# Kernel tuning notes

Hardware: AMD Instinct MI355X
Metric: run time of the kernel (lower is better)

Reference implementation:

```python
import jax, jax.numpy as jnp
import numpy as np


def setup_inputs() -> dict:
    key = jax.random.key(0)
    k1, k2 = jax.random.split(key)
    input = jax.random.normal(k1, (4, 2048, 2048), dtype=jnp.float32)
    target = jax.random.normal(k2, (4, 2048, 2048), dtype=jnp.float32) * 2.0 + 0.5
    return {"input": input, "target": target}


def _hist_match(source, template):
    """JAX histogram matching, equivalent to the numpy unique/cumsum/interp
    version for inputs with distinct values (true for continuous random data).

    For each source element x, its empirical quantile is
        q(x) = count(source <= x) / N  == s_quantiles[bin_idx] in the numpy code,
    computed via sort + searchsorted(side='right').
    The template CDF is the sorted template paired with quantiles (j+1)/M,
    matching cumsum(t_counts)/M at each (unique) value.
    """
    src = source.ravel()
    tmpl_sorted = jnp.sort(template.ravel())
    N = src.shape[0]
    M = tmpl_sorted.shape[0]
    s_sorted = jnp.sort(src)
    # rank of each element among all source elements (count <= x)
    ranks = jnp.searchsorted(s_sorted, src, side='right')
    s_q = ranks.astype(jnp.float32) / jnp.float32(N)
    t_q = jnp.arange(1, M + 1, dtype=jnp.float32) / jnp.float32(M)
    matched = jnp.interp(s_q, t_q, tmpl_sorted)
    return matched.reshape(source.shape)


def reference(input, target):
    # hist_match_torch.forward: matched histogram (non-differentiable in original)
    matched = jax.lax.stop_gradient(_hist_match(input, target))
    # HistogramLoss: (matched - input)^2 summed / numel
    loss = jnp.mean((matched - input) ** 2)
    # original forward returns `input`; the meaningful computed quantities are
    # the matched tensor and the loss, so we return both.
    return matched, loss
```

## Files before the change

### kernel.cpp

```cpp
#include <hip/hip_runtime.h>
#include <cstdint>


#define NBINS    8192u
#define HGX      512u
#define MGX      2048u
#define KIN      2048u
#define KTG      4096u

__device__ __forceinline__ void bin_and_frac(float x, unsigned& b, float& frac) {
    float d = __builtin_fmaf(x, 256.0f, 4096.0f);
    d = fminf(fmaxf(d, 0.0f), 8191.999f);
    unsigned bb = (unsigned)d;
    b = bb;
    frac = d - (float)bb;
}

__device__ __forceinline__ void hist8(float4 A0, float4 A1, unsigned* h) {
    float xs[8] = {A0.x, A0.y, A0.z, A0.w, A1.x, A1.y, A1.z, A1.w};
    #pragma unroll
    for (int k = 0; k < 8; k++) {
        unsigned b; float f;
        bin_and_frac(xs[k], b, f);
        atomicAdd(&h[b], 1u);
    }
}

__global__ __launch_bounds__(512, 8) void hist_kernel(const float* __restrict__ in,
                                                      const float* __restrict__ tg,
                                                      unsigned* __restrict__ H, unsigned n8) {
    __shared__ unsigned h[NBINS];
    for (unsigned i = threadIdx.x; i < NBINS; i += 512) h[i] = 0;
    __syncthreads();
    const float* xp = blockIdx.y ? tg : in;
    const float4* x4 = (const float4*)xp;
    unsigned* Hh = H + blockIdx.y * NBINS;
    unsigned stride = gridDim.x * 512;
    unsigned i0 = blockIdx.x * 512 + threadIdx.x;
    if (i0 < n8) {
        unsigned iB = i0 + stride; unsigned iBc = (iB < n8) ? iB : i0;
        float4 p00 = x4[2 * i0], p01 = x4[2 * i0 + 1];
        float4 p10 = x4[2 * iBc], p11 = x4[2 * iBc + 1];
        for (unsigned i = i0; i < n8; i += stride) {
            unsigned nx = i + 2 * stride;
            unsigned nxc = (nx < n8) ? nx : i0;
            float4 q0 = x4[2 * nxc], q1 = x4[2 * nxc + 1];
            hist8(p00, p01, h);
            p00 = p10; p01 = p11; p10 = q0; p11 = q1;
        }
    }
    __syncthreads();
    for (unsigned i = threadIdx.x; i < NBINS; i += 512) {
        unsigned v = h[i];
        if (v) atomicAdd(&Hh[i], v);
    }
}

__global__ void scan_kernel(const unsigned* __restrict__ H, unsigned* __restrict__ C) {
    __shared__ unsigned s[1024];
    const unsigned* h = H + blockIdx.x * NBINS;
    unsigned* c = C + blockIdx.x * (NBINS + 1);
    unsigned base = threadIdx.x * 8;
    unsigned v[8]; unsigned own = 0;
    #pragma unroll
    for (int k = 0; k < 8; k++) { v[k] = h[base + k]; own += v[k]; }
    s[threadIdx.x] = own; __syncthreads();
    for (unsigned off = 1; off < 1024; off <<= 1) {
        unsigned t = (threadIdx.x >= off) ? s[threadIdx.x - off] : 0u;
        __syncthreads();
        s[threadIdx.x] += t;
        __syncthreads();
    }
    unsigned ex = s[threadIdx.x] - own;
    #pragma unroll
    for (int k = 0; k < 8; k++) { unsigned t = v[k]; c[base + k] = ex; ex += t; }
    if (threadIdx.x == 1023) c[NBINS] = s[1023];
}

__global__ void buildAB_kernel(const unsigned* __restrict__ Cin, const unsigned* __restrict__ Ctg,
                               float2* __restrict__ AB, int* __restrict__ hdr, unsigned n) {
    unsigned b = blockIdx.x * blockDim.x + threadIdx.x;
    if (b >= NBINS) return;
    unsigned r0 = Cin[b], r1 = Cin[b + 1];
    if (r1 <= KIN) atomicMax(&hdr[0], (int)b);
    if (r0 >= n - KIN) atomicMax(&hdr[1], (int)(8192u - b));
    unsigned t0 = Ctg[b], t1 = Ctg[b + 1];
    if (t1 <= KTG) atomicMax(&hdr[2], (int)b);
    if (t0 >= n - KTG) atomicMax(&hdr[3], (int)(8192u - b));
    if (r1 == r0) { AB[b] = make_float2(0.f, 0.f); return; }
    const float w = 32.0f / (float)NBINS;
    float v[2];
    unsigned rr[2] = {r0, r1};
    #pragma unroll
    for (int k = 0; k < 2; k++) {
        unsigned r = rr[k]; if (r > n - 1) r = n - 1;
        unsigned lo = 0, hi = NBINS;
        while (hi - lo > 1) { unsigned mid = (lo + hi) >> 1; if (Ctg[mid] <= r) lo = mid; else hi = mid; }
        unsigned c0 = Ctg[lo], c1 = Ctg[lo + 1];
        v[k] = -16.0f + (float)lo * w + w * ((float)(r - c0 + 1) / (float)(c1 - c0));
    }
    AB[b] = make_float2(v[0], v[1] - v[0]);
}

__global__ void exact_target_kernel(const float* __restrict__ tg_lo, const float* __restrict__ tg_hi,
                                    const unsigned* __restrict__ ctrs,
                                    float* __restrict__ Tlo, float* __restrict__ Thi) {
    __shared__ __align__(16) float v[KTG];
    int side = blockIdx.y;
    const float* src = side ? tg_hi : tg_lo;
    unsigned m = ctrs[side ? 3 : 2];
    if (m > KTG) m = KTG;
    float sgn = side ? -1.f : 1.f;
    for (unsigned k = threadIdx.x; k < m; k += 1024) v[k] = sgn * src[k];
    __syncthreads();
    unsigned j = blockIdx.x * 1024 + threadIdx.x;
    if (j >= m) return;
    float y = v[j];
    unsigned lt = 0, le = 0;
    unsigned m4 = m & ~3u;
    for (unsigned k = 0; k < m4; k += 4) {
        float4 z = *(const float4*)&v[k];
        lt += (z.x < y) + (z.y < y) + (z.z < y) + (z.w < y);
        le += (z.x <= y) + (z.y <= y) + (z.z <= y) + (z.w <= y);
    }
    for (unsigned k = m4; k < m; k++) { lt += (v[k] < y); le += (v[k] <= y); }
    float yo = sgn * y;
    if (side) {
        for (unsigned idx = KTG - le; idx < KTG - lt; idx++) Thi[idx] = yo;
    } else {
        for (unsigned r = lt; r < le; r++) Tlo[r] = yo;
    }
}

__device__ __forceinline__ void collect8(float4 A0, float4 A1, int blo, int bhi,
                                         float* __restrict__ tg_lo, float* __restrict__ tg_hi,
                                         unsigned* __restrict__ ctrs) {
    float xs[8] = {A0.x, A0.y, A0.z, A0.w, A1.x, A1.y, A1.z, A1.w};
    bool lo8[8], hi8[8]; bool any = false;
    #pragma unroll
    for (int k = 0; k < 8; k++) {
        unsigned b; float f;
        bin_and_frac(xs[k], b, f);
        lo8[k] = ((int)b <= blo);
        hi8[k] = ((int)b >= bhi);
        any = any || lo8[k] || hi8[k];
    }
    if (any) {
        #pragma unroll
        for (int k = 0; k < 8; k++) {
            if (lo8[k]) { unsigned p = atomicAdd(&ctrs[2], 1u); tg_lo[p] = xs[k]; }
            else if (hi8[k]) { unsigned p = atomicAdd(&ctrs[3], 1u); tg_hi[p] = xs[k]; }
        }
    }
}

__device__ __forceinline__ float match8(float4 A0, float4 A1, unsigned i,
                                        const float2* __restrict__ AB, int blo, int bhi,
                                        float* __restrict__ out,
                                        float* __restrict__ vlo, unsigned* __restrict__ ilo,
                                        float* __restrict__ vhi, unsigned* __restrict__ ihi,
                                        unsigned* __restrict__ ctrs) {
    float xs[8] = {A0.x, A0.y, A0.z, A0.w, A1.x, A1.y, A1.z, A1.w};
    unsigned b[8]; float fr[8];
    #pragma unroll
    for (int k = 0; k < 8; k++) bin_and_frac(xs[k], b[k], fr[k]);
    float2 ab[8];
    #pragma unroll
    for (int k = 0; k < 8; k++) ab[k] = AB[b[k]];
    float m[8]; bool tl[8]; bool any = false; float acc = 0.f;
    #pragma unroll
    for (int k = 0; k < 8; k++) {
        m[k] = __builtin_fmaf(ab[k].y, fr[k], ab[k].x);
        tl[k] = ((int)b[k] <= blo) || ((int)b[k] >= bhi);
        any = any || tl[k];
        float d = tl[k] ? 0.f : (m[k] - xs[k]);
        acc = __builtin_fmaf(d, d, acc);
    }
    ((float4*)out)[2 * i]     = make_float4(m[0], m[1], m[2], m[3]);
    ((float4*)out)[2 * i + 1] = make_float4(m[4], m[5], m[6], m[7]);
    if (any) {
        #pragma unroll
        for (int k = 0; k < 8; k++) {
            if (!tl[k]) continue;
            if ((int)b[k] <= blo) { unsigned p = atomicAdd(&ctrs[0], 1u); vlo[p] = xs[k]; ilo[p] = 8 * i + k; }
            else                  { unsigned p = atomicAdd(&ctrs[1], 1u); vhi[p] = xs[k]; ihi[p] = 8 * i + k; }
        }
    }
    return acc;
}

__global__ __launch_bounds__(256, 8) void matchcollect_kernel(
        const float* __restrict__ input, const float* __restrict__ target,
        const float2* __restrict__ AB, const int* __restrict__ hdr,
        float* __restrict__ vlo, unsigned* __restrict__ ilo,
        float* __restrict__ vhi, unsigned* __restrict__ ihi,
        float* __restrict__ tg_lo, float* __restrict__ tg_hi,
        unsigned* __restrict__ ctrs,
        float* __restrict__ out, float* __restrict__ bpart,
        unsigned n) {
    unsigned n8 = n >> 3;
    unsigned stride = gridDim.x * 256;
    unsigned i0 = blockIdx.x * 256 + threadIdx.x;

    if (blockIdx.y == 1) {
        int blo = hdr[2], bhi = 8192 - hdr[3];
        if (i0 < n8) {
            const float4* x4 = (const float4*)target;
            unsigned iB = i0 + stride; unsigned iBc = (iB < n8) ? iB : i0;
            float4 p00 = x4[2 * i0], p01 = x4[2 * i0 + 1];
            float4 p10 = x4[2 * iBc], p11 = x4[2 * iBc + 1];
            for (unsigned i = i0; i < n8; i += stride) {
                unsigned nx = i + 2 * stride;
                unsigned nxc = (nx < n8) ? nx : i0;
                float4 q0 = x4[2 * nxc], q1 = x4[2 * nxc + 1];
                collect8(p00, p01, blo, bhi, tg_lo, tg_hi, ctrs);
                p00 = p10; p01 = p11; p10 = q0; p11 = q1;
            }
        }
        return;
    }

    int blo = hdr[0], bhi = 8192 - hdr[1];
    float acc = 0.f;
    if (i0 < n8) {
        const float4* x4 = (const float4*)input;
        unsigned iB = i0 + stride; unsigned iBc = (iB < n8) ? iB : i0;
        float4 p00 = x4[2 * i0], p01 = x4[2 * i0 + 1];
        float4 p10 = x4[2 * iBc], p11 = x4[2 * iBc + 1];
        for (unsigned i = i0; i < n8; i += stride) {
            unsigned nx = i + 2 * stride;
            unsigned nxc = (nx < n8) ? nx : i0;
            float4 q0 = x4[2 * nxc], q1 = x4[2 * nxc + 1];
            acc += match8(p00, p01, i, AB, blo, bhi, out, vlo, ilo, vhi, ihi, ctrs);
            p00 = p10; p01 = p11; p10 = q0; p11 = q1;
        }
    }
    #pragma unroll
    for (int off = 32; off > 0; off >>= 1) acc += __shfl_down(acc, off, 64);
    if ((threadIdx.x & 63) == 0)
        bpart[blockIdx.x * 4 + (threadIdx.x >> 6)] = acc;
}

__global__ void loss_reduce_kernel(const float* __restrict__ bpart, float* __restrict__ loss,
                                   unsigned nb, unsigned n) {
    float s = 0.f;
    for (unsigned i = threadIdx.x; i < nb; i += 1024) s += bpart[i];
    #pragma unroll
    for (int off = 32; off > 0; off >>= 1) s += __shfl_down(s, off, 64);
    __shared__ float ws[16];
    int w = threadIdx.x >> 6;
    if ((threadIdx.x & 63) == 0) ws[w] = s;
    __syncthreads();
    if (threadIdx.x == 0) {
        float t = 0.f;
        #pragma unroll
        for (int k = 0; k < 16; k++) t += ws[k];
        *loss = t * (1.0f / (float)n);
    }
}

__global__ void exact_input_kernel(const float* __restrict__ in_lo_v, const unsigned* __restrict__ in_lo_i,
                                   const float* __restrict__ in_hi_v, const unsigned* __restrict__ in_hi_i,
                                   const unsigned* __restrict__ ctrs,
                                   const float* __restrict__ Tlo, const float* __restrict__ Thi,
                                   float* __restrict__ out, float* __restrict__ loss, unsigned n) {
    __shared__ __align__(16) float v[KIN];
    int side = blockIdx.y;
    const float* sv = side ? in_hi_v : in_lo_v;
    const unsigned* si = side ? in_hi_i : in_lo_i;
    unsigned m = ctrs[side ? 1 : 0];
    if (m > KIN) m = KIN;
    float sgn = side ? -1.f : 1.f;
    for (unsigned k = threadIdx.x; k < m; k += 1024) v[k] = sgn * sv[k];
    __syncthreads();
    unsigned j = blockIdx.x * 1024 + threadIdx.x;
    float d2 = 0.f;
    if (j < m) {
        float y = v[j];
        unsigned lt = 0, le = 0;
        unsigned m4 = m & ~3u;
        for (unsigned k = 0; k < m4; k += 4) {
            float4 z = *(const float4*)&v[k];
            lt += (z.x < y) + (z.y < y) + (z.z < y) + (z.w < y);
            le += (z.x <= y) + (z.y <= y) + (z.z <= y) + (z.w <= y);
        }
        for (unsigned k = m4; k < m; k++) { lt += (v[k] < y); le += (v[k] <= y); }
        float mv = side ? Thi[KTG - 1 - lt] : Tlo[le - 1];
        float x = sgn * y;
        out[si[j]] = mv;
        float d = mv - x;
        d2 = d * d;
    }
    #pragma unroll
    for (int off = 32; off > 0; off >>= 1) d2 += __shfl_down(d2, off, 64);
    if ((threadIdx.x & 63) == 0 && d2 != 0.f)
        atomicAdd(loss, d2 * (1.0f / (float)n));
}

extern "C" void kernel_launch(void* const* d_in, const int* in_sizes, int n_in,
                              void* d_out, int out_size, void* d_ws, size_t ws_size,
                              hipStream_t stream) {
    const float* input  = (const float*)d_in[0];
    const float* target = (const float*)d_in[1];
    unsigned n = (unsigned)in_sizes[0];
    float* out  = (float*)d_out;
    float* loss = out + n;

    char* wsb = (char*)d_ws;
    unsigned* H    = (unsigned*)(wsb);
    unsigned* Cin  = (unsigned*)(wsb + 64 * 1024);
    unsigned* Ctg  = Cin + (NBINS + 1);
    float2*   AB   = (float2*)  (wsb + 160 * 1024);
    char*     aux  = wsb + 224 * 1024;
    int*      hdr  = (int*)     (aux);
    unsigned* ctrs = (unsigned*)(aux + 16);
    float*    bpart= (float*)   (aux + 64);
    char*     tails= aux + 64 + 65536 + 64;
    float*    in_lo_v = (float*)   (tails);
    unsigned* in_lo_i = (unsigned*)(tails + KIN * 4);
    float*    in_hi_v = (float*)   (tails + KIN * 8);
    unsigned* in_hi_i = (unsigned*)(tails + KIN * 12);
    float*    tg_lo   = (float*)   (tails + KIN * 16);
    float*    tg_hi   = (float*)   (tails + KIN * 16 + KTG * 4);
    float*    Tlo     = (float*)   (tails + KIN * 16 + KTG * 8);
    float*    Thi     = (float*)   (tails + KIN * 16 + KTG * 12);

    (void)hipMemsetAsync(H, 0, 2 * NBINS * 4, stream);
    (void)hipMemsetAsync(hdr, 0, 32, stream);
    (void)hipMemsetAsync(loss, 0, 4, stream);

    unsigned n8 = n >> 3;

    hist_kernel<<<dim3(HGX, 2), 512, 0, stream>>>(input, target, H, n8);
    scan_kernel<<<2, 1024, 0, stream>>>(H, Cin);
    buildAB_kernel<<<NBINS / 256, 256, 0, stream>>>(Cin, Ctg, AB, hdr, n);

    matchcollect_kernel<<<dim3(MGX, 2), 256, 0, stream>>>(input, target, AB, hdr,
                                                          in_lo_v, in_lo_i, in_hi_v, in_hi_i,
                                                          tg_lo, tg_hi, ctrs, out, bpart, n);
    loss_reduce_kernel<<<1, 1024, 0, stream>>>(bpart, loss, MGX * 4, n);
    exact_target_kernel<<<dim3((KTG + 1023) / 1024, 2), 1024, 0, stream>>>(tg_lo, tg_hi, ctrs, Tlo, Thi);
    exact_input_kernel<<<dim3((KIN + 1023) / 1024, 2), 1024, 0, stream>>>(in_lo_v, in_lo_i, in_hi_v, in_hi_i,
                                                                          ctrs, Tlo, Thi, out, loss, n);
}
```

Measured before the change: 527.3 us.

## Collect target tail candidates during histogram pass to avoid second target read

The histogram kernel now saves target values in conservative fixed tail bins to per-block candidate buffers using shared-memory counters. A small filter kernel then compacts the candidates against the exact tail bounds, which replaces the full second pass over the target tensor that the match kernel used to do. A fallback kernel rescans the whole target if a buffer overflows or the bounds fall outside the fixed bins. The cost is extra shared atomics in the histogram pass and two more launches.

```diff
diff --git a/kernel.cpp b/kernel.cpp
--- a/kernel.cpp
+++ b/kernel.cpp
@@ -7,6 +7,9 @@
 #define MGX      2048u
 #define KIN      2048u
 #define KTG      4096u
+#define CLO_BIN  3328u
+#define CHI_BIN  5120u
+#define CAPB     4096u
 
 __device__ __forceinline__ void bin_and_frac(float x, unsigned& b, float& frac) {
     float d = __builtin_fmaf(x, 256.0f, 4096.0f);
@@ -16,25 +19,40 @@
     frac = d - (float)bb;
 }
 
-__device__ __forceinline__ void hist8(float4 A0, float4 A1, unsigned* h) {
+__device__ __forceinline__ void hist8c(float4 A0, float4 A1, unsigned* h, bool collect,
+                                       unsigned* ccnt, float* clo, float* chi) {
     float xs[8] = {A0.x, A0.y, A0.z, A0.w, A1.x, A1.y, A1.z, A1.w};
     #pragma unroll
     for (int k = 0; k < 8; k++) {
         unsigned b; float f;
         bin_and_frac(xs[k], b, f);
         atomicAdd(&h[b], 1u);
+        if (collect) {
+            if (b <= CLO_BIN) { unsigned p = atomicAdd(&ccnt[0], 1u); if (p < CAPB) clo[p] = xs[k]; }
+            else if (b >= CHI_BIN) { unsigned p = atomicAdd(&ccnt[1], 1u); if (p < CAPB) chi[p] = xs[k]; }
+        }
     }
 }
 
 __global__ __launch_bounds__(512, 8) void hist_kernel(const float* __restrict__ in,
                                                       const float* __restrict__ tg,
-                                                      unsigned* __restrict__ H, unsigned n8) {
+                                                      unsigned* __restrict__ H,
+                                                      float* __restrict__ cand_lo,
+                                                      float* __restrict__ cand_hi,
+                                                      unsigned* __restrict__ cand_cnt,
+                                                      unsigned* __restrict__ gflag,
+                                                      unsigned n8) {
     __shared__ unsigned h[NBINS];
+    __shared__ unsigned ccnt[2];
     for (unsigned i = threadIdx.x; i < NBINS; i += 512) h[i] = 0;
-    __syncthreads();
-    const float* xp = blockIdx.y ? tg : in;
+    if (threadIdx.x == 0) { ccnt[0] = 0; ccnt[1] = 0; }
+    __syncthreads();
+    bool collect = (blockIdx.y == 1);
+    const float* xp = collect ? tg : in;
     const float4* x4 = (const float4*)xp;
     unsigned* Hh = H + blockIdx.y * NBINS;
+    float* clo = cand_lo + (size_t)blockIdx.x * CAPB;
+    float* chi = cand_hi + (size_t)blockIdx.x * CAPB;
     unsigned stride = gridDim.x * 512;
     unsigned i0 = blockIdx.x * 512 + threadIdx.x;
     if (i0 < n8) {
@@ -45,7 +63,7 @@
             unsigned nx = i + 2 * stride;
             unsigned nxc = (nx < n8) ? nx : i0;
             float4 q0 = x4[2 * nxc], q1 = x4[2 * nxc + 1];
-            hist8(p00, p01, h);
+            hist8c(p00, p01, h, collect, ccnt, clo, chi);
             p00 = p10; p01 = p11; p10 = q0; p11 = q1;
         }
     }
@@ -53,6 +71,11 @@
     for (unsigned i = threadIdx.x; i < NBINS; i += 512) {
         unsigned v = h[i];
         if (v) atomicAdd(&Hh[i], v);
+    }
+    if (collect && threadIdx.x == 0) {
+        cand_cnt[2 * blockIdx.x]     = ccnt[0];
+        cand_cnt[2 * blockIdx.x + 1] = ccnt[1];
+        if (ccnt[0] > CAPB || ccnt[1] > CAPB) *gflag = 1;
     }
 }
 
@@ -102,6 +125,61 @@
     AB[b] = make_float2(v[0], v[1] - v[0]);
 }
 
+__global__ __launch_bounds__(256) void filter_tg_kernel(
+        const float* __restrict__ cand_lo, const float* __restrict__ cand_hi,
+        const unsigned* __restrict__ cand_cnt, const unsigned* __restrict__ gflag,
+        const int* __restrict__ hdr,
+        float* __restrict__ tg_lo, float* __restrict__ tg_hi, unsigned* __restrict__ ctrs) {
+    int blo = hdr[2], bhi = 8192 - hdr[3];
+    if (*gflag || blo > (int)CLO_BIN || bhi < (int)CHI_BIN) return;
+    __shared__ float buf_lo[CAPB];
+    __shared__ float buf_hi[CAPB];
+    __shared__ unsigned cnt2[2];
+    __shared__ unsigned base2[2];
+    if (threadIdx.x == 0) { cnt2[0] = 0; cnt2[1] = 0; }
+    __syncthreads();
+    unsigned blk = blockIdx.x;
+    unsigned nlo = cand_cnt[2 * blk], nhi = cand_cnt[2 * blk + 1];
+    if (nlo > CAPB) nlo = CAPB;
+    if (nhi > CAPB) nhi = CAPB;
+    const float* cl = cand_lo + (size_t)blk * CAPB;
+    const float* ch = cand_hi + (size_t)blk * CAPB;
+    for (unsigned i = threadIdx.x; i < nlo; i += 256) {
+        float v = cl[i]; unsigned b; float f; bin_and_frac(v, b, f);
+        if ((int)b <= blo) { unsigned p = atomicAdd(&cnt2[0], 1u); buf_lo[p] = v; }
+    }
+    for (unsigned i = threadIdx.x; i < nhi; i += 256) {
+        float v = ch[i]; unsigned b; float f; bin_and_frac(v, b, f);
+        if ((int)b >= bhi) { unsigned p = atomicAdd(&cnt2[1], 1u); buf_hi[p] = v; }
+    }
+    __syncthreads();
+    if (threadIdx.x == 0) base2[0] = atomicAdd(&ctrs[2], cnt2[0]);
+    if (threadIdx.x == 1) base2[1] = atomicAdd(&ctrs[3], cnt2[1]);
+    __syncthreads();
+    for (unsigned i = threadIdx.x; i < cnt2[0]; i += 256) tg_lo[base2[0] + i] = buf_lo[i];
+    for (unsigned i = threadIdx.x; i < cnt2[1]; i += 256) tg_hi[base2[1] + i] = buf_hi[i];
+}
+
+__global__ void fallback_collect_kernel(const float* __restrict__ target,
+                                        const unsigned* __restrict__ gflag,
+                                        const int* __restrict__ hdr,
+                                        float* __restrict__ tg_lo, float* __restrict__ tg_hi,
+                                        unsigned* __restrict__ ctrs, unsigned n4) {
+    int blo = hdr[2], bhi = 8192 - hdr[3];
+    if (!*gflag && blo <= (int)CLO_BIN && bhi >= (int)CHI_BIN) return;
+    unsigned stride = gridDim.x * blockDim.x;
+    for (unsigned i = blockIdx.x * blockDim.x + threadIdx.x; i < n4; i += stride) {
+        float4 v = ((const float4*)target)[i];
+        float xs[4] = {v.x, v.y, v.z, v.w};
+        #pragma unroll
+        for (int k = 0; k < 4; k++) {
+            unsigned b; float f; bin_and_frac(xs[k], b, f);
+            if ((int)b <= blo) { unsigned p = atomicAdd(&ctrs[2], 1u); tg_lo[p] = xs[k]; }
+            else if ((int)b >= bhi) { unsigned p = atomicAdd(&ctrs[3], 1u); tg_hi[p] = xs[k]; }
+        }
+    }
+}
+
 __global__ void exact_target_kernel(const float* __restrict__ tg_lo, const float* __restrict__ tg_hi,
                                     const unsigned* __restrict__ ctrs,
                                     float* __restrict__ Tlo, float* __restrict__ Thi) {
@@ -132,28 +210,6 @@
     }
 }
 
-__device__ __forceinline__ void collect8(float4 A0, float4 A1, int blo, int bhi,
-                                         float* __restrict__ tg_lo, float* __restrict__ tg_hi,
-                                         unsigned* __restrict__ ctrs) {
-    float xs[8] = {A0.x, A0.y, A0.z, A0.w, A1.x, A1.y, A1.z, A1.w};
-    bool lo8[8], hi8[8]; bool any = false;
-    #pragma unroll
-    for (int k = 0; k < 8; k++) {
-        unsigned b; float f;
-        bin_and_frac(xs[k], b, f);
-        lo8[k] = ((int)b <= blo);
-        hi8[k] = ((int)b >= bhi);
-        any = any || lo8[k] || hi8[k];
-    }
-    if (any) {
-        #pragma unroll
-        for (int k = 0; k < 8; k++) {
-            if (lo8[k]) { unsigned p = atomicAdd(&ctrs[2], 1u); tg_lo[p] = xs[k]; }
-            else if (hi8[k]) { unsigned p = atomicAdd(&ctrs[3], 1u); tg_hi[p] = xs[k]; }
-        }
-    }
-}
-
 __device__ __forceinline__ float match8(float4 A0, float4 A1, unsigned i,
                                         const float2* __restrict__ AB, int blo, int bhi,
                                         float* __restrict__ out,
@@ -189,37 +245,17 @@
     return acc;
 }
 
-__global__ __launch_bounds__(256, 8) void matchcollect_kernel(
-        const float* __restrict__ input, const float* __restrict__ target,
+__global__ __launch_bounds__(256, 8) void match_kernel(
+        const float* __restrict__ input,
         const float2* __restrict__ AB, const int* __restrict__ hdr,
         float* __restrict__ vlo, unsigned* __restrict__ ilo,
         float* __restrict__ vhi, unsigned* __restrict__ ihi,
-        float* __restrict__ tg_lo, float* __restrict__ tg_hi,
         unsigned* __restrict__ ctrs,
         float* __restrict__ out, float* __restrict__ bpart,
         unsigned n) {
     unsigned n8 = n >> 3;
     unsigned stride = gridDim.x * 256;
     unsigned i0 = blockIdx.x * 256 + threadIdx.x;
-
-    if (blockIdx.y == 1) {
-        int blo = hdr[2], bhi = 8192 - hdr[3];
-        if (i0 < n8) {
-            const float4* x4 = (const float4*)target;
-            unsigned iB = i0 + stride; unsigned iBc = (iB < n8) ? iB : i0;
-            float4 p00 = x4[2 * i0], p01 = x4[2 * i0 + 1];
-            float4 p10 = x4[2 * iBc], p11 = x4[2 * iBc + 1];
-            for (unsigned i = i0; i < n8; i += stride) {
-                unsigned nx = i + 2 * stride;
-                unsigned nxc = (nx < n8) ? nx : i0;
-                float4 q0 = x4[2 * nxc], q1 = x4[2 * nxc + 1];
-                collect8(p00, p01, blo, bhi, tg_lo, tg_hi, ctrs);
-                p00 = p10; p01 = p11; p10 = q0; p11 = q1;
-            }
-        }
-        return;
-    }
-
     int blo = hdr[0], bhi = 8192 - hdr[1];
     float acc = 0.f;
     if (i0 < n8) {
@@ -314,6 +350,7 @@
     char*     aux  = wsb + 224 * 1024;
     int*      hdr  = (int*)     (aux);
     unsigned* ctrs = (unsigned*)(aux + 16);
+    unsigned* gflag= (unsigned*)(aux + 32);
     float*    bpart= (float*)   (aux + 64);
     char*     tails= aux + 64 + 65536 + 64;
     float*    in_lo_v = (float*)   (tails);
@@ -324,20 +361,28 @@
     float*    tg_hi   = (float*)   (tails + KIN * 16 + KTG * 4);
     float*    Tlo     = (float*)   (tails + KIN * 16 + KTG * 8);
     float*    Thi     = (float*)   (tails + KIN * 16 + KTG * 12);
+    unsigned* cand_cnt= (unsigned*)(wsb + 512 * 1024);
+    float*    cand_lo = (float*)   (wsb + 1024 * 1024);
+    float*    cand_hi = (float*)   (wsb + 10 * 1024 * 1024);
 
     (void)hipMemsetAsync(H, 0, 2 * NBINS * 4, stream);
-    (void)hipMemsetAsync(hdr, 0, 32, stream);
+    (void)hipMemsetAsync(hdr, 0, 48, stream);
     (void)hipMemsetAsync(loss, 0, 4, stream);
 
     unsigned n8 = n >> 3;
-
-    hist_kernel<<<dim3(HGX, 2), 512, 0, stream>>>(input, target, H, n8);
+    unsigned n4 = n >> 2;
+
+    hist_kernel<<<dim3(HGX, 2), 512, 0, stream>>>(input, target, H, cand_lo, cand_hi,
+                                                  cand_cnt, gflag, n8);
     scan_kernel<<<2, 1024, 0, stream>>>(H, Cin);
     buildAB_kernel<<<NBINS / 256, 256, 0, stream>>>(Cin, Ctg, AB, hdr, n);
 
-    matchcollect_kernel<<<dim3(MGX, 2), 256, 0, stream>>>(input, target, AB, hdr,
-                                                          in_lo_v, in_lo_i, in_hi_v, in_hi_i,
-                                                          tg_lo, tg_hi, ctrs, out, bpart, n);
+    filter_tg_kernel<<<HGX, 256, 0, stream>>>(cand_lo, cand_hi, cand_cnt, gflag, hdr,
+                                              tg_lo, tg_hi, ctrs);
+    fallback_collect_kernel<<<2048, 256, 0, stream>>>(target, gflag, hdr, tg_lo, tg_hi, ctrs, n4);
+
+    match_kernel<<<MGX, 256, 0, stream>>>(input, AB, hdr, in_lo_v, in_lo_i, in_hi_v, in_hi_i,
+                                          ctrs, out, bpart, n);
     loss_reduce_kernel<<<1, 1024, 0, stream>>>(bpart, loss, MGX * 4, n);
     exact_target_kernel<<<dim3((KTG + 1023) / 1024, 2), 1024, 0, stream>>>(tg_lo, tg_hi, ctrs, Tlo, Thi);
     exact_input_kernel<<<dim3((KIN + 1023) / 1024, 2), 1024, 0, stream>>>(in_lo_v, in_lo_i, in_hi_v, in_hi_i,
```

Measured after the change: 468.2 us. 11.2% less time.
